# Kernel tuning notes

Measured on AMD Instinct MI355X. Metric: run time of the kernel, lower is better.

## Reference

```python
import jax, jax.numpy as jnp
import numpy as np
from jax.scipy.special import logsumexp

V, C, S, H = 32000, 4096, 32, 512
B, T = 32, 256
NEG = jnp.float32(-1e10)  # masked_fill value used by mask_emission


def _res(x, w1, b1, w2, b2):
    # ResidualLayerOld: relu(lin1(x)); relu(lin2(h) + x)
    h = jax.nn.relu(x @ w1.T + b1)
    return jax.nn.relu(h @ w2.T + b2 + x)


def setup_inputs() -> dict:
    key = jax.random.key(0)
    ks = jax.random.split(key, 16)
    g = lambda i, shape, s=0.02: jax.random.normal(ks[i], shape, jnp.float32) * s
    return {
        "text": jax.random.randint(ks[0], (B, T), 0, V),
        "word2state": jax.random.randint(ks[1], (V, S), 0, C - 1),
        "start_emb": g(2, (C, H), 1.0),
        "start_w1": g(3, (H, H)), "start_b1": jnp.zeros((H,), jnp.float32),
        "start_w2": g(4, (H, H)), "start_b2": jnp.zeros((H,), jnp.float32),
        "start_w3": g(5, (1, H)), "start_b3": jnp.zeros((1,), jnp.float32),
        "state_emb": g(6, (C, H), 1.0),
        "trans_w1": g(7, (H, H)), "trans_b1": jnp.zeros((H,), jnp.float32),
        "trans_w2": g(8, (H, H)), "trans_b2": jnp.zeros((H,), jnp.float32),
        "next_state_proj": g(9, (C, H)),
        "preterminal_emb": g(10, (C, H), 1.0),
        "term_w1": g(11, (H, H)), "term_b1": jnp.zeros((H,), jnp.float32),
        "term_w2": g(12, (H, H)), "term_b2": jnp.zeros((H,), jnp.float32),
        "term_w3": g(13, (V, H)), "term_b3": jnp.zeros((V,), jnp.float32),
    }


def _forward(text, word2state, start_emb, start_w1, start_b1, start_w2, start_b2,
             start_w3, start_b3, state_emb, trans_w1, trans_b1, trans_w2, trans_b2,
             next_state_proj, preterminal_emb, term_w1, term_b1, term_w2, term_b2,
             term_w3, term_b3):
    ninf = -jnp.inf
    # start distribution over states [C]
    start = jax.nn.log_softmax(
        (_res(start_emb, start_w1, start_b1, start_w2, start_b2) @ start_w3.T + start_b3)[:, 0])
    # transition [C, C]: mask last column, row-normalize, mask last row (pad state)
    tl = _res(state_emb, trans_w1, trans_b1, trans_w2, trans_b2) @ next_state_proj.T
    tl = tl.at[:, -1].set(ninf)
    trans = jax.nn.log_softmax(tl, axis=-1)
    trans = jnp.where(jnp.isnan(trans), ninf, trans)
    trans = trans.at[-1, :].set(ninf)
    # emission [C, V]: sparse word2state mask, normalize over vocab
    el = _res(preterminal_emb, term_w1, term_b1, term_w2, term_b2) @ term_w3.T + term_b3
    emask = jnp.zeros((C, V), bool).at[
        word2state.reshape(-1), jnp.repeat(jnp.arange(V), S)].set(True)
    emit = jax.nn.log_softmax(jnp.where(emask, el, NEG), axis=-1)
    emit = jnp.where(jnp.isnan(emit), ninf, emit)
    emit = emit.at[-1, :].set(ninf)
    # clamp to the S states allowed for each observed word
    cs = word2state[text]                                  # [B, T, S]
    pot = trans[cs[:, :-1, :, None], cs[:, 1:, None, :]]   # [B, T-1, S, S] (cur, next)
    obs = emit[cs, text[:, :, None]]                       # [B, T, S]
    init = start[cs[:, 0]]                                 # [B, S]
    pot = pot + obs[:, 1:, None, :]                        # obs at t+1 on next axis
    pot = pot.at[:, 0].add(init[:, :, None] + obs[:, 0, :, None])
    pot = jnp.swapaxes(pot, -1, -2)                        # [B, T-1, next, prev]
    # log-domain forward scan (the fb kernel's alpha recursion)
    alpha0 = logsumexp(pot[:, 0], axis=-1)                 # [B, S]
    def step(alpha, p):
        return logsumexp(p + alpha[:, None, :], axis=-1), None
    alpha, _ = jax.lax.scan(step, alpha0, jnp.swapaxes(pot[:, 1:], 0, 1))
    return logsumexp(alpha, axis=-1).sum()                 # evidence (sum over batch)


def reference(text, word2state, start_emb, start_w1, start_b1, start_w2, start_b2,
              start_w3, start_b3, state_emb, trans_w1, trans_b1, trans_w2, trans_b2,
              next_state_proj, preterminal_emb, term_w1, term_b1, term_w2, term_b2,
              term_w3, term_b3):
    return _forward(text, word2state, start_emb, start_w1, start_b1, start_w2,
                    start_b2, start_w3, start_b3, state_emb, trans_w1, trans_b1,
                    trans_w2, trans_b2, next_state_proj, preterminal_emb, term_w1,
                    term_b1, term_w2, term_b2, term_w3, term_b3)
```

## Files before the change

kernel.cpp:

```cpp
#include <hip/hip_runtime.h>
#include <hip/hip_bf16.h>
#include <math.h>

#define NV 32000
#define NC 4096
#define NS 32
#define NH 512
#define NB 32
#define NT 256

typedef short s16x8 __attribute__((ext_vector_type(8)));
typedef float f32x4 __attribute__((ext_vector_type(4)));

__device__ __forceinline__ float wredMax(float v){
  #pragma unroll
  for (int o = 32; o; o >>= 1) v = fmaxf(v, __shfl_xor(v, o, 64));
  return v;
}
__device__ __forceinline__ float wredSum(float v){
  #pragma unroll
  for (int o = 32; o; o >>= 1) v += __shfl_xor(v, o, 64);
  return v;
}
__device__ __forceinline__ int f2ord(float f){ int i = __float_as_int(f); return i >= 0 ? i : (i ^ 0x7fffffff); }
__device__ __forceinline__ float ord2f(int i){ return __int_as_float(i >= 0 ? i : (i ^ 0x7fffffff)); }

__device__ __forceinline__ unsigned short f2bf(float x){
  unsigned int u = __float_as_uint(x);
  return (unsigned short)((u + 0x7fffu + ((u >> 16) & 1u)) >> 16);
}
__device__ __forceinline__ float bf2f(unsigned short h){
  return __uint_as_float((unsigned int)h << 16);
}

__device__ __forceinline__ void conv_body(const float* __restrict__ src,
                                          unsigned short* __restrict__ dst, int idx)
{
  const float* s = src + (size_t)idx * 8;
  float4 f0 = *(const float4*)s;
  float4 f1 = *(const float4*)(s + 4);
  float fv[8] = {f0.x, f0.y, f0.z, f0.w, f1.x, f1.y, f1.z, f1.w};
  s16x8 vh, vl;
  #pragma unroll
  for (int e = 0; e < 8; ++e) {
    unsigned short h = f2bf(fv[e]);
    vh[e] = (short)h;
    vl[e] = (short)f2bf(fv[e] - bf2f(h));
  }
  int r = idx >> 6, c8 = idx & 63;
  unsigned short* d = dst + (size_t)r * 1024 + c8 * 8;
  *(s16x8*)d = vh;
  *(s16x8*)(d + 512) = vl;
}

struct ConvArgs {
  const float* src[10];
  unsigned short* dst[10];
  int rows[10];
};

__global__ __launch_bounds__(256)
void conv_batch(ConvArgs a)
{
  int z = blockIdx.y;
  int idx = blockIdx.x * 256 + threadIdx.x;
  if (idx >= a.rows[z] * 64) return;
  conv_body(a.src[z], a.dst[z], idx);
}

__global__ __launch_bounds__(256)
void conv_single(const float* __restrict__ src, unsigned short* __restrict__ dst)
{
  int idx = blockIdx.x * 256 + threadIdx.x;
  conv_body(src, dst, idx);
}

template<int BM, bool RELU, bool BIAS, bool RES>
__global__ __launch_bounds__(256)
void gemm_bf16s(const unsigned short* __restrict__ Asp, const unsigned short* __restrict__ Bsp,
                const float* __restrict__ bias, const float* __restrict__ res,
                float* __restrict__ Co, int M, int N, int K)
{
  constexpr int BN = 128;
  constexpr int MF = BM / 32;
  constexpr int NFR = 4;
  __shared__ char smem[BM * 128 + BN * 128];
  char* smA = smem;
  char* smB = smem + BM * 128;

  const int tid  = threadIdx.x;
  const int lane = tid & 63, w = tid >> 6;
  const int wr = w >> 1, wc = w & 1;
  const int bm = blockIdx.y * BM, bn = blockIdx.x * BN;
  const int lda = 2 * K;
  const int l8 = lane >> 3, s8 = lane & 7;
  const int frow = lane & 15, kgrp = lane >> 4;

  f32x4 acc[MF][NFR] = {};

  #pragma unroll 1
  for (int seg = 0; seg < 3; ++seg) {
    const int aoff = (seg == 1) ? K : 0;
    const int boff = (seg == 2) ? K : 0;
    #pragma unroll 1
    for (int k0 = 0; k0 < K; k0 += 64) {
      #pragma unroll
      for (int c = 0; c < MF; ++c) {
        int q = w * MF + c;
        int row = q * 8 + l8;
        s16x8 v = *(const s16x8*)(Asp + (size_t)(bm + row) * lda + aoff + k0 + s8 * 8);
        unsigned int o = (unsigned int)(row * 128 + (s8 << 4));
        o ^= (unsigned int)((row & 7) << 4);
        *(s16x8*)(smA + o) = v;
      }
      #pragma unroll
      for (int c = 0; c < NFR; ++c) {
        int q = w * NFR + c;
        int row = q * 8 + l8;
        s16x8 v = *(const s16x8*)(Bsp + (size_t)(bn + row) * lda + boff + k0 + s8 * 8);
        unsigned int o = (unsigned int)(row * 128 + (s8 << 4));
        o ^= (unsigned int)((row & 7) << 4);
        *(s16x8*)(smB + o) = v;
      }
      __syncthreads();
      #pragma unroll
      for (int kk = 0; kk < 64; kk += 32) {
        s16x8 af[MF], bfr[NFR];
        #pragma unroll
        for (int im = 0; im < MF; ++im) {
          int ar = wr * (BM / 2) + im * 16 + frow;
          unsigned int o = ((unsigned int)(ar * 128 + (kk + kgrp * 8) * 2)) ^ ((unsigned int)((ar & 7) << 4));
          af[im] = *(const s16x8*)(smA + o);
        }
        #pragma unroll
        for (int jn = 0; jn < NFR; ++jn) {
          int bc = wc * 64 + jn * 16 + frow;
          unsigned int o = ((unsigned int)(bc * 128 + (kk + kgrp * 8) * 2)) ^ ((unsigned int)((bc & 7) << 4));
          bfr[jn] = *(const s16x8*)(smB + o);
        }
        #pragma unroll
        for (int im = 0; im < MF; ++im)
          #pragma unroll
          for (int jn = 0; jn < NFR; ++jn)
            asm volatile("v_mfma_f32_16x16x32_bf16 %0, %1, %2, %0"
                         : "+v"(acc[im][jn]) : "v"(af[im]), "v"(bfr[jn]));
      }
      __syncthreads();
    }
  }
  asm volatile("s_nop 7\n\ts_nop 7" ::: );
  #pragma unroll
  for (int im = 0; im < MF; ++im) {
    int row0 = bm + wr * (BM / 2) + im * 16 + kgrp * 4;
    #pragma unroll
    for (int jn = 0; jn < NFR; ++jn) {
      int col = bn + wc * 64 + jn * 16 + frow;
      #pragma unroll
      for (int j = 0; j < 4; ++j) {
        int r = row0 + j;
        float v = acc[im][jn][j];
        if constexpr (BIAS) v += bias[col];
        if constexpr (RES)  v += res[(size_t)r * N + col];
        if constexpr (RELU) v = fmaxf(v, 0.f);
        Co[(size_t)r * N + col] = v;
      }
    }
  }
}

__global__ __launch_bounds__(64)
void dot_head(const float* __restrict__ hS, const float* __restrict__ w3,
              const float* __restrict__ b3, float* __restrict__ sv)
{
  int c = blockIdx.x, lane = threadIdx.x;
  const float* hrow = hS + (size_t)c * NH;
  float acc = 0.f;
  #pragma unroll
  for (int e = 0; e < 8; ++e) acc += hrow[lane + e*64] * w3[lane + e*64];
  acc = wredSum(acc);
  if (lane == 0) sv[c] = acc + b3[0];
}

__global__ __launch_bounds__(1024)
void lse_vec(const float* __restrict__ x, int n, float* __restrict__ out)
{
  int tid = threadIdx.x;
  __shared__ float sm[16], ss[16];
  float m = -INFINITY;
  for (int i = tid; i < n; i += 1024) m = fmaxf(m, x[i]);
  m = wredMax(m);
  if ((tid & 63) == 0) sm[tid >> 6] = m;
  __syncthreads();
  m = sm[0];
  #pragma unroll
  for (int wv = 1; wv < 16; ++wv) m = fmaxf(m, sm[wv]);
  float s = 0.f;
  for (int i = tid; i < n; i += 1024) s += expf(x[i] - m);
  s = wredSum(s);
  if ((tid & 63) == 0) ss[tid >> 6] = s;
  __syncthreads();
  if (tid == 0) {
    float tot = 0.f;
    #pragma unroll
    for (int wv = 0; wv < 16; ++wv) tot += ss[wv];
    out[0] = m + logf(tot);
  }
}

__global__ __launch_bounds__(256)
void row_lse_trans(const float* __restrict__ tl, float* __restrict__ lse_t)
{
  int c = blockIdx.x;
  const float* row = tl + (size_t)c * NC;
  int tid = threadIdx.x;
  __shared__ float sm[4], ss[4];
  float m = -INFINITY;
  for (int n = tid; n < NC - 1; n += 256) m = fmaxf(m, row[n]);
  m = wredMax(m);
  if ((tid & 63) == 0) sm[tid >> 6] = m;
  __syncthreads();
  m = fmaxf(fmaxf(sm[0], sm[1]), fmaxf(sm[2], sm[3]));
  float s = 0.f;
  for (int n = tid; n < NC - 1; n += 256) s += expf(row[n] - m);
  s = wredSum(s);
  if ((tid & 63) == 0) ss[tid >> 6] = s;
  __syncthreads();
  if (tid == 0) lse_t[c] = m + logf(ss[0] + ss[1] + ss[2] + ss[3]);
}

__global__ __launch_bounds__(256)
void el_kernel(const int* __restrict__ w2s, const float* __restrict__ hP,
               const float* __restrict__ w3, const float* __restrict__ b3,
               float* __restrict__ el_g, unsigned int* __restrict__ vmask)
{
  int v = blockIdx.x;
  __shared__ float w3v[NH];
  __shared__ int crow[NS];
  int tid = threadIdx.x;
  if (tid < NS) crow[tid] = w2s[(size_t)v * NS + tid];
  for (int e = tid; e < NH; e += 256) w3v[e] = w3[(size_t)v * NH + e];
  __syncthreads();
  if (tid < 64) {
    bool valid = false;
    if (tid < NS) {
      valid = true;
      int c = crow[tid];
      for (int s2 = 0; s2 < tid; ++s2) if (crow[s2] == c) { valid = false; break; }
    }
    unsigned long long bal = __ballot(valid);
    if (tid == 0) vmask[v] = (unsigned int)(bal & 0xffffffffull);
  }
  int wave = tid >> 6, lane = tid & 63;
  float b3v = b3[v];
  #pragma unroll
  for (int q = 0; q < 8; ++q) {
    int s = wave * 8 + q;
    int c = crow[s];
    const float* hrow = hP + (size_t)c * NH;
    float acc = 0.f;
    #pragma unroll
    for (int e = 0; e < 8; ++e) acc += hrow[lane + e*64] * w3v[lane + e*64];
    acc = wredSum(acc);
    if (lane == 0) el_g[(size_t)v * NS + s] = acc + b3v;
  }
}

__global__ __launch_bounds__(256)
void init_e(int* __restrict__ emax, unsigned long long* __restrict__ esum)
{
  int i = blockIdx.x * 256 + threadIdx.x;
  if (i < NC) { emax[i] = 0x80000000; esum[i] = 0ull; }
}
__global__ __launch_bounds__(256)
void emit_max_k(const int* __restrict__ w2s, const float* __restrict__ el_g,
                const unsigned int* __restrict__ vmask, int* __restrict__ emax)
{
  int idx = blockIdx.x * 256 + threadIdx.x;
  int v = idx >> 5, s = idx & 31;
  if (!((vmask[v] >> s) & 1u)) return;
  atomicMax(&emax[w2s[idx]], f2ord(el_g[idx]));
}
__global__ __launch_bounds__(256)
void emit_sum_k(const int* __restrict__ w2s, const float* __restrict__ el_g,
                const unsigned int* __restrict__ vmask, const int* __restrict__ emax,
                unsigned long long* __restrict__ esum)
{
  int idx = blockIdx.x * 256 + threadIdx.x;
  int v = idx >> 5, s = idx & 31;
  if (!((vmask[v] >> s) & 1u)) return;
  int c = w2s[idx];
  float p = expf(el_g[idx] - ord2f(emax[c]));
  atomicAdd(&esum[c], (unsigned long long)(p * 0x1p40f));
}
__global__ __launch_bounds__(256)
void emit_fin_k(const int* __restrict__ emax, const unsigned long long* __restrict__ esum,
                float* __restrict__ lse_e)
{
  int c = blockIdx.x * 256 + threadIdx.x;
  if (c < NC) lse_e[c] = ord2f(emax[c]) + logf((float)esum[c] * 0x1p-40f);
}

__global__ __launch_bounds__(1024)
void scan_kernel(const int* __restrict__ text, const int* __restrict__ w2s,
                 const float* __restrict__ tl, const float* __restrict__ lse_t,
                 const float* __restrict__ sv, const float* __restrict__ lse_st,
                 const float* __restrict__ el_g, const float* __restrict__ lse_e,
                 float* __restrict__ out_b)
{
  int b = blockIdx.x;
  __shared__ unsigned short cs[NT][NS];
  __shared__ float D[NT][NS];
  __shared__ float beta[NS];
  __shared__ float alpha_out[NS];
  __shared__ int textb[NT];
  int tid = threadIdx.x;

  if (tid < NT) textb[tid] = text[b * NT + tid];
  __syncthreads();
  for (int idx = tid; idx < NT * NS; idx += 1024) {
    int t = idx >> 5, s = idx & 31;
    int v = textb[t];
    int c = w2s[v * NS + s];
    cs[t][s] = (unsigned short)c;
    D[t][s] = el_g[(size_t)v * NS + s] - lse_e[c] - lse_t[c];
  }
  __syncthreads();
  if (tid < NS) {
    int c0 = cs[0][tid];
    beta[tid] = sv[c0] - lse_st[0] + D[0][tid];
  }
  __syncthreads();

  const int j = tid >> 5, i = tid & 31;
  float val_next = tl[(size_t)cs[0][i] * NC + cs[1][j]];
  for (int t = 0; t < NT - 1; ++t) {
    float val = val_next;
    if (t < NT - 2) val_next = tl[(size_t)cs[t+1][i] * NC + cs[t+2][j]];
    float x = val + beta[i];
    float m = x;
    #pragma unroll
    for (int o = 16; o; o >>= 1) m = fmaxf(m, __shfl_xor(m, o, 32));
    float p = expf(x - m);
    #pragma unroll
    for (int o = 16; o; o >>= 1) p += __shfl_xor(p, o, 32);
    float r = m + logf(p);
    __syncthreads();
    if (i == 0) {
      if (t < NT - 2) beta[j] = r + D[t+1][j];
      else alpha_out[j] = r + D[t+1][j] + lse_t[cs[t+1][j]];
    }
    __syncthreads();
  }

  if (tid < 32) {
    float a = alpha_out[tid];
    float m = a;
    #pragma unroll
    for (int o = 16; o; o >>= 1) m = fmaxf(m, __shfl_xor(m, o, 32));
    float p = expf(a - m);
    #pragma unroll
    for (int o = 16; o; o >>= 1) p += __shfl_xor(p, o, 32);
    if (tid == 0) out_b[b] = m + logf(p);
  }
}

__global__ void final_sum(const float* __restrict__ out_b, float* __restrict__ out)
{
  if (threadIdx.x == 0) {
    float s = 0.f;
    for (int b = 0; b < NB; ++b) s += out_b[b];
    out[0] = s;
  }
}

extern "C" void kernel_launch(void* const* d_in, const int* in_sizes, int n_in,
                              void* d_out, int out_size, void* d_ws, size_t ws_size,
                              hipStream_t stream)
{
  (void)in_sizes; (void)n_in; (void)out_size; (void)ws_size;
  const int*   text      = (const int*)d_in[0];
  const int*   w2s       = (const int*)d_in[1];
  const float* start_emb = (const float*)d_in[2];
  const float* start_w1  = (const float*)d_in[3];
  const float* start_b1  = (const float*)d_in[4];
  const float* start_w2  = (const float*)d_in[5];
  const float* start_b2  = (const float*)d_in[6];
  const float* start_w3  = (const float*)d_in[7];
  const float* start_b3  = (const float*)d_in[8];
  const float* state_emb = (const float*)d_in[9];
  const float* trans_w1  = (const float*)d_in[10];
  const float* trans_b1  = (const float*)d_in[11];
  const float* trans_w2  = (const float*)d_in[12];
  const float* trans_b2  = (const float*)d_in[13];
  const float* nsp       = (const float*)d_in[14];
  const float* pre_emb   = (const float*)d_in[15];
  const float* term_w1   = (const float*)d_in[16];
  const float* term_b1   = (const float*)d_in[17];
  const float* term_w2   = (const float*)d_in[18];
  const float* term_b2   = (const float*)d_in[19];
  const float* term_w3   = (const float*)d_in[20];
  const float* term_b3   = (const float*)d_in[21];

  float* tl    = (float*)d_ws;
  float* h1    = tl + 16777216;
  float* h2    = h1 + 2097152;
  float* sv    = h2 + 2097152;
  float* lse_t = sv + NC;
  float* lse_e = lse_t + NC;
  float* lse_s = lse_e + NC;
  float* out_b = lse_s + 64;
  float* el_g  = out_b + 64;
  unsigned int* vmask = (unsigned int*)(el_g + 1024000);
  int* emax    = (int*)(vmask + 32000);
  unsigned long long* esum = (unsigned long long*)(emax + 4096);
  unsigned short* sE_s  = (unsigned short*)(esum + 4096);
  unsigned short* tE_s  = sE_s  + 4194304;
  unsigned short* pE_s  = tE_s  + 4194304;
  unsigned short* nsp_s = pE_s  + 4194304;
  unsigned short* h1_s  = nsp_s + 4194304;
  unsigned short* w1S_s = h1_s  + 4194304;
  unsigned short* w2S_s = w1S_s + 524288;
  unsigned short* w1T_s = w2S_s + 524288;
  unsigned short* w2T_s = w1T_s + 524288;
  unsigned short* w1P_s = w2T_s + 524288;
  unsigned short* w2P_s = w1P_s + 524288;
  unsigned short* h2t_s = sE_s;

  ConvArgs ca;
  ca.src[0]=start_emb; ca.dst[0]=sE_s;  ca.rows[0]=NC;
  ca.src[1]=state_emb; ca.dst[1]=tE_s;  ca.rows[1]=NC;
  ca.src[2]=pre_emb;   ca.dst[2]=pE_s;  ca.rows[2]=NC;
  ca.src[3]=nsp;       ca.dst[3]=nsp_s; ca.rows[3]=NC;
  ca.src[4]=start_w1;  ca.dst[4]=w1S_s; ca.rows[4]=NH;
  ca.src[5]=start_w2;  ca.dst[5]=w2S_s; ca.rows[5]=NH;
  ca.src[6]=trans_w1;  ca.dst[6]=w1T_s; ca.rows[6]=NH;
  ca.src[7]=trans_w2;  ca.dst[7]=w2T_s; ca.rows[7]=NH;
  ca.src[8]=term_w1;   ca.dst[8]=w1P_s; ca.rows[8]=NH;
  ca.src[9]=term_w2;   ca.dst[9]=w2P_s; ca.rows[9]=NH;
  conv_batch<<<dim3(1024, 10), 256, 0, stream>>>(ca);

  dim3 blk(256);
  dim3 gHH(4, 64);
  dim3 gCC(32, 32);

  gemm_bf16s<64, true,  true,  false><<<gHH, blk, 0, stream>>>(sE_s, w1S_s, start_b1, nullptr,   h1, NC, NH, NH);
  conv_single<<<1024, 256, 0, stream>>>(h1, h1_s);
  gemm_bf16s<64, true,  true,  true ><<<gHH, blk, 0, stream>>>(h1_s, w2S_s, start_b2, start_emb, h2, NC, NH, NH);
  dot_head<<<NC, 64, 0, stream>>>(h2, start_w3, start_b3, sv);
  lse_vec<<<1, 1024, 0, stream>>>(sv, NC, lse_s);

  gemm_bf16s<64, true,  true,  false><<<gHH, blk, 0, stream>>>(tE_s, w1T_s, trans_b1, nullptr,   h1, NC, NH, NH);
  conv_single<<<1024, 256, 0, stream>>>(h1, h1_s);
  gemm_bf16s<64, true,  true,  true ><<<gHH, blk, 0, stream>>>(h1_s, w2T_s, trans_b2, state_emb, h2, NC, NH, NH);
  conv_single<<<1024, 256, 0, stream>>>(h2, h2t_s);
  gemm_bf16s<128, false, false, false><<<gCC, blk, 0, stream>>>(h2t_s, nsp_s, nullptr, nullptr, tl, NC, NC, NH);
  row_lse_trans<<<NC, 256, 0, stream>>>(tl, lse_t);

  gemm_bf16s<64, true,  true,  false><<<gHH, blk, 0, stream>>>(pE_s, w1P_s, term_b1, nullptr,  h1, NC, NH, NH);
  conv_single<<<1024, 256, 0, stream>>>(h1, h1_s);
  gemm_bf16s<64, true,  true,  true ><<<gHH, blk, 0, stream>>>(h1_s, w2P_s, term_b2, pre_emb,  h2, NC, NH, NH);
  el_kernel<<<NV, 256, 0, stream>>>(w2s, h2, term_w3, term_b3, el_g, vmask);
  init_e<<<16, 256, 0, stream>>>(emax, esum);
  emit_max_k<<<NV * NS / 256, 256, 0, stream>>>(w2s, el_g, vmask, emax);
  emit_sum_k<<<NV * NS / 256, 256, 0, stream>>>(w2s, el_g, vmask, emax, esum);
  emit_fin_k<<<NC / 256, 256, 0, stream>>>(emax, esum, lse_e);

  scan_kernel<<<NB, 1024, 0, stream>>>(text, w2s, tl, lse_t, sv, lse_s, el_g, lse_e, out_b);
  final_sum<<<1, 64, 0, stream>>>(out_b, (float*)d_out);
}
```

Baseline: 1.058 ms.

## Pregather transition potentials in a parallel kernel before the serial scan

After: 959.5 us. 1.1x faster.

```diff
diff --git a/kernel.cpp b/kernel.cpp
--- a/kernel.cpp
+++ b/kernel.cpp
@@ -300,9 +300,36 @@
   if (c < NC) lse_e[c] = ord2f(emax[c]) + logf((float)esum[c] * 0x1p-40f);
 }
 
+__global__ __launch_bounds__(256)
+void build_cs(const int* __restrict__ text, const int* __restrict__ w2s,
+              unsigned short* __restrict__ cs_all)
+{
+  int idx = blockIdx.x * 256 + threadIdx.x;
+  int s = idx & 31;
+  int bt = idx >> 5;
+  int v = text[bt];
+  cs_all[idx] = (unsigned short)w2s[(size_t)v * NS + s];
+}
+
+__global__ __launch_bounds__(1024)
+void gather_pot(const unsigned short* __restrict__ cs_all, const float* __restrict__ tl,
+                float* __restrict__ pot)
+{
+  int t = blockIdx.x;
+  int b = blockIdx.y;
+  int tid = threadIdx.x;
+  __shared__ unsigned short c1s[NS], c2s[NS];
+  if (tid < NS) c1s[tid] = cs_all[((size_t)b * NT + t) * NS + tid];
+  else if (tid < 2 * NS) c2s[tid - NS] = cs_all[((size_t)b * NT + t + 1) * NS + (tid - NS)];
+  __syncthreads();
+  int gi = tid >> 5, gj = tid & 31;
+  float v = tl[(size_t)c1s[gi] * NC + c2s[gj]];
+  pot[((size_t)b * (NT - 1) + t) * 1024 + gj * 32 + gi] = v;
+}
+
 __global__ __launch_bounds__(1024)
 void scan_kernel(const int* __restrict__ text, const int* __restrict__ w2s,
-                 const float* __restrict__ tl, const float* __restrict__ lse_t,
+                 const float* __restrict__ pot, const float* __restrict__ lse_t,
                  const float* __restrict__ sv, const float* __restrict__ lse_st,
                  const float* __restrict__ el_g, const float* __restrict__ lse_e,
                  float* __restrict__ out_b)
@@ -332,10 +359,11 @@
   __syncthreads();
 
   const int j = tid >> 5, i = tid & 31;
-  float val_next = tl[(size_t)cs[0][i] * NC + cs[1][j]];
+  const float* potb = pot + (size_t)b * (NT - 1) * 1024;
+  float val_next = potb[tid];
   for (int t = 0; t < NT - 1; ++t) {
     float val = val_next;
-    if (t < NT - 2) val_next = tl[(size_t)cs[t+1][i] * NC + cs[t+2][j]];
+    if (t < NT - 2) val_next = potb[(size_t)(t + 1) * 1024 + tid];
     float x = val + beta[i];
     float m = x;
     #pragma unroll
@@ -424,7 +452,9 @@
   unsigned short* w2T_s = w1T_s + 524288;
   unsigned short* w1P_s = w2T_s + 524288;
   unsigned short* w2P_s = w1P_s + 524288;
+  unsigned short* cs_all = w2P_s + 524288;
   unsigned short* h2t_s = sE_s;
+  float* pot = (float*)sE_s;
 
   ConvArgs ca;
   ca.src[0]=start_emb; ca.dst[0]=sE_s;  ca.rows[0]=NC;
@@ -465,6 +495,9 @@
   emit_sum_k<<<NV * NS / 256, 256, 0, stream>>>(w2s, el_g, vmask, emax, esum);
   emit_fin_k<<<NC / 256, 256, 0, stream>>>(emax, esum, lse_e);
 
-  scan_kernel<<<NB, 1024, 0, stream>>>(text, w2s, tl, lse_t, sv, lse_s, el_g, lse_e, out_b);
+  build_cs<<<NB * NT * NS / 256, 256, 0, stream>>>(text, w2s, cs_all);
+  gather_pot<<<dim3(NT - 1, NB), 1024, 0, stream>>>(cs_all, tl, pot);
+
+  scan_kernel<<<NB, 1024, 0, stream>>>(text, w2s, pot, lse_t, sv, lse_s, el_g, lse_e, out_b);
   final_sum<<<1, 64, 0, stream>>>(out_b, (float*)d_out);
 }
```
